# Performance work log

Measured on AMD Instinct MI355X. Metric: run time of the kernel, lower is better.

The kernel has to match this reference:

```python
import jax, jax.numpy as jnp
import numpy as np

B, C, H, W = 8, 96, 256, 256
PATCH, DIM, HEAD = 2, 384, 4
D = DIM // HEAD          # 96, minGRU feature dim
K = 2 * PATCH + 1        # 5, patch-embed kernel
GK = 3                   # positional conv kernel


def setup_inputs() -> dict:
    key = jax.random.key(0)
    ks = jax.random.split(key, 16)
    w = lambda k, shape: jax.random.normal(k, shape, jnp.float32) * 0.02
    return {
        'x': jax.random.normal(ks[0], (B, C, H, W), jnp.float32),
        'r_pw': w(ks[1], (DIM, C, K, K)),            # Conv2d weight (out,in,kh,kw)
        'r_pb': w(ks[2], (DIM,)),
        'c_pw': w(ks[3], (DIM, C, K, K)),
        'c_pb': w(ks[4], (DIM,)),
        'r_pe_w': w(ks[5], (DIM, DIM // C, GK, GK)),  # grouped conv, groups=C
        'r_pe_b': w(ks[6], (DIM,)),
        'c_pe_w': w(ks[7], (DIM, DIM // C, GK, GK)),
        'c_pe_b': w(ks[8], (DIM,)),
        'r_un_w': w(ks[9], (DIM, C, PATCH, PATCH)),   # ConvTranspose2d weight (in,out,kh,kw)
        'r_un_b': w(ks[10], (C,)),
        'c_un_w': w(ks[11], (DIM, C, PATCH, PATCH)),
        'c_un_b': w(ks[12], (C,)),
        'r_gru_w': w(ks[13], (D, 2 * D)),             # minGRU to_hidden_and_gate (no bias)
        'c_gru_w': w(ks[14], (D, 2 * D)),
    }


def _conv(x, w, b, stride, pad, groups=1):
    y = jax.lax.conv_general_dilated(
        x, w, (stride, stride), [(pad, pad), (pad, pad)],
        dimension_numbers=('NCHW', 'OIHW', 'NCHW'), feature_group_count=groups)
    return y + b[None, :, None, None]


def _min_gru(seq, w):
    # seq: (N, S, D); log-space parallel scan (heinsen scan), lucidrains minGRU
    hg = seq @ w                                  # (N, S, 2D)
    hidden, gate = jnp.split(hg, 2, axis=-1)
    log_coeffs = -jax.nn.softplus(gate)           # log(1 - z)
    log_z = -jax.nn.softplus(-gate)               # log z
    log_tilde_h = jnp.where(hidden >= 0,
                            jnp.log(jax.nn.relu(hidden) + 0.5),
                            -jax.nn.softplus(-hidden))
    a_star = jnp.cumsum(log_coeffs, axis=1)
    log_h = a_star + jax.lax.cumlogsumexp(log_z + log_tilde_h - a_star, axis=1)
    return jnp.exp(log_h)


def _unpatch(x, w, b):
    # ConvTranspose2d with kernel==stride==PATCH, pad=0: pure block expansion
    Bq, Ci, Hp, Wp = x.shape
    y = jnp.einsum('bchw,copq->bohpwq', x, w).reshape(Bq, w.shape[1], Hp * PATCH, Wp * PATCH)
    return y + b[None, :, None, None]


def reference(x, r_pw, r_pb, c_pw, c_pb, r_pe_w, r_pe_b, c_pe_w, c_pe_b,
              r_un_w, r_un_b, c_un_w, c_un_b, r_gru_w, c_gru_w):
    r = _conv(x, r_pw, r_pb, PATCH, PATCH)        # (B, DIM, Hp, Wp)
    c = _conv(x, c_pw, c_pb, PATCH, PATCH)
    r_pe = _conv(r, r_pe_w, r_pe_b, 1, 1, groups=C)
    c_pe = _conv(c, c_pe_w, c_pe_b, 1, 1, groups=C)
    Bq, _, Hp, Wp = r.shape
    # row scan: (B,head,D,Hp,Wp) -> (B,head,Wp,Hp,D) -> scan over Hp
    r = r.reshape(Bq, HEAD, D, Hp, Wp).transpose(0, 1, 4, 3, 2).reshape(-1, Hp, D)
    # col scan: (B,head,D,Hp,Wp) -> (B,head,Hp,Wp,D) -> scan over Wp
    c = c.reshape(Bq, HEAD, D, Hp, Wp).transpose(0, 1, 3, 4, 2).reshape(-1, Wp, D)
    r = _min_gru(r, r_gru_w)
    c = _min_gru(c, c_gru_w)
    r = r.reshape(Bq, HEAD, Wp, Hp, D).transpose(0, 1, 4, 3, 2).reshape(Bq, DIM, Hp, Wp)
    c = c.reshape(Bq, HEAD, Hp, Wp, D).transpose(0, 1, 4, 2, 3).reshape(Bq, DIM, Hp, Wp)
    return _unpatch(r + r_pe, r_un_w, r_un_b) + _unpatch(c + c_pe, c_un_w, c_un_b)
```

## Files before the change

kernel.cpp:

```cpp
#include <hip/hip_runtime.h>
#include <stdint.h>
#include <stdio.h>

typedef __attribute__((ext_vector_type(8))) short short8;
typedef __attribute__((ext_vector_type(4))) float f32x4;
typedef __attribute__((ext_vector_type(2))) float f32x2;
typedef __attribute__((ext_vector_type(4))) unsigned int u32x4;
typedef __attribute__((ext_vector_type(4))) unsigned short u16x4;

#define DEV static __device__ __forceinline__

DEV unsigned short f2bf(float f){
  unsigned u = __float_as_uint(f);
  u += 0x7FFFu + ((u >> 16) & 1u);
  return (unsigned short)(u >> 16);
}
DEV float bf2f(unsigned short h){ return __uint_as_float(((unsigned)h) << 16); }

__global__ __launch_bounds__(256) void k_xt(const float* __restrict__ x,
                                            unsigned short* __restrict__ xt){
  int bid = blockIdx.x;
  int wq = bid & 3, h = (bid >> 2) & 255, b = bid >> 10;
  int w0 = wq * 64;
  __shared__ unsigned short s[64 * 104];
  int t = threadIdx.x;
  int wl = t & 63, cq = t >> 6;
  const float* xp = x + ((size_t)b * 96 * 256 + h) * 256 + w0 + wl;
  #pragma unroll
  for (int i = 0; i < 24; ++i){
    int c = cq + i * 4;
    s[wl * 104 + c] = f2bf(xp[(size_t)c * 65536]);
  }
  __syncthreads();
  unsigned short* dst = xt + (((size_t)b * 260 + h + 2) * 260 + (w0 + 2)) * 128;
  #pragma unroll
  for (int p = 0; p < 3; ++p){
    int i = t + p * 256;
    int w = i / 12, ch = i % 12;
    u32x4 v = *(const u32x4*)&s[w * 104 + ch * 8];
    *(u32x4*)&dst[(size_t)w * 128 + ch * 8] = v;
  }
}

__global__ __launch_bounds__(256) void k_pack(const float* __restrict__ rpw, const float* __restrict__ cpw,
    const float* __restrict__ runw, const float* __restrict__ cunw,
    const float* __restrict__ runb, const float* __restrict__ cunb,
    const float* __restrict__ rgw,  const float* __restrict__ cgw,
    unsigned short* __restrict__ A2, unsigned short* __restrict__ Aun,
    unsigned short* __restrict__ Agr, float* __restrict__ bun){
  int tid = blockIdx.x * 256 + threadIdx.x;
  const int NA2 = 768 * 2400, NUN = 384 * 768, NGR = 2 * 192 * 96;
  if (tid < NA2){
    int oc = tid / 2400, r = tid % 2400;
    int kh = r / 480, kw = (r / 96) % 5, ic = r % 96;
    const float* W = oc < 384 ? rpw : cpw;
    int o = oc < 384 ? oc : oc - 384;
    A2[tid] = f2bf(W[(((size_t)o * 96 + ic) * 5 + kh) * 5 + kw]);
  } else if (tid < NA2 + NUN){
    int i = tid - NA2;
    int m = i / 768, ci = i % 768;
    int co = m >> 2, p = (m >> 1) & 1, q = m & 1;
    const float* W = ci < 384 ? runw : cunw;
    int c = ci < 384 ? ci : ci - 384;
    Aun[i] = f2bf(W[(((size_t)c * 96 + co) * 2 + p) * 2 + q]);
  } else if (tid < NA2 + NUN + NGR){
    int i = tid - NA2 - NUN;
    int side = i / 18432, r = i % 18432;
    int m = r / 96, k = r % 96;
    const float* W = side ? cgw : rgw;
    Agr[i] = f2bf(W[k * 192 + m]);
  } else if (tid < NA2 + NUN + NGR + 96){
    int co = tid - NA2 - NUN - NGR;
    bun[co] = runb[co] + cunb[co];
  }
}

__global__ __launch_bounds__(512) void k_conv(const unsigned short* __restrict__ xt,
    const unsigned short* __restrict__ A2,
    const float* __restrict__ rpb, const float* __restrict__ cpb,
    unsigned short* __restrict__ cl){
  __shared__ char lds[160768];
  const int BOFF = 26624;
  const int BPITCH = 33536;
  const int BITEMS = 8384;
  int t = threadIdx.x, lane = t & 63;
  int wid = t >> 6, mw = wid >> 2, nw = wid & 3;
  int wl = lane & 15, cg = lane >> 4;
  int bid = blockIdx.x;
  int xcd = bid & 7, rr = bid >> 3;
  int mt = rr % 6, pgrp = rr / 6;
  int p = pgrp * 8 + xcd;
  int wq = p & 1, hq = (p >> 1) & 31, b = p >> 6;
  int ho0 = hq * 4, wo0 = wq * 64;
  int M0 = mt * 128;

  int a_oc = t >> 2, a_q = t & 3;
  const unsigned short* Aoc = A2 + (size_t)(M0 + a_oc) * 2400 + a_q * 24;
  char* Adst = lds + a_oc * 208 + a_q * 48;

  f32x4 acc[4][4];
  #pragma unroll
  for (int i = 0; i < 4; ++i)
    #pragma unroll
    for (int j = 0; j < 4; ++j) acc[i][j] = (f32x4){0.f, 0.f, 0.f, 0.f};

  u32x4 aR[3], bR[17];
  #pragma unroll
  for (int c = 0; c < 3; ++c) aR[c] = *(const u32x4*)(Aoc + c * 8);
  #pragma unroll
  for (int it = 0; it < 17; ++it){
    int i = t + it * 512;
    if (i < BITEMS){
      int row = i / 2096, j = i % 2096, col = j >> 4, ch = j & 15;
      bR[it] = *(const u32x4*)&xt[(((size_t)b * 260 + 2 * ho0 + 2 * row) * 260 + 2 * wo0 + col) * 128 + ch * 8];
    }
  }
  #pragma unroll
  for (int c = 0; c < 3; ++c) *(u32x4*)(Adst + c * 16) = aR[c];
  #pragma unroll
  for (int it = 0; it < 17; ++it){
    int i = t + it * 512;
    if (i < BITEMS){
      int row = i / 2096, j = i % 2096, col = j >> 4, ch = j & 15;
      *(u32x4*)(lds + BOFF + row * BPITCH + col * 256 + (ch ^ ((col >> 1) & 7)) * 16) = bR[it];
    }
  }
  __syncthreads();

  for (int kh = 0; kh < 5; ++kh){
    #pragma unroll
    for (int kw = 0; kw < 5; ++kw){
      bool last = (kh == 4 && kw == 4);
      bool khb  = (kw == 4 && kh < 4);
      if (!last){
        int nkh = kh + (kw == 4 ? 1 : 0), nkw = (kw == 4 ? 0 : kw + 1);
        const unsigned short* As = Aoc + (nkh * 5 + nkw) * 96;
        #pragma unroll
        for (int c = 0; c < 3; ++c) aR[c] = *(const u32x4*)(As + c * 8);
      }
      if (khb){
        #pragma unroll
        for (int it = 0; it < 17; ++it){
          int i = t + it * 512;
          if (i < BITEMS){
            int row = i / 2096, j = i % 2096, col = j >> 4, ch = j & 15;
            bR[it] = *(const u32x4*)&xt[(((size_t)b * 260 + 2 * ho0 + 2 * row + kh + 1) * 260 + 2 * wo0 + col) * 128 + ch * 8];
          }
        }
      }
      {
        int col = 32 * nw + 2 * wl + kw;
        int sx = (col >> 1) & 7;
        #pragma unroll
        for (int ics = 0; ics < 3; ++ics){
          short8 af[4], bfr[4];
          #pragma unroll
          for (int mf = 0; mf < 4; ++mf)
            af[mf] = *(const short8*)(lds + (mw * 64 + mf * 16 + wl) * 208 + ics * 64 + cg * 16);
          int chl = (ics * 4 + cg) ^ sx;
          #pragma unroll
          for (int nf = 0; nf < 4; ++nf)
            bfr[nf] = *(const short8*)(lds + BOFF + nf * BPITCH + col * 256 + chl * 16);
          #pragma unroll
          for (int mf = 0; mf < 4; ++mf)
            #pragma unroll
            for (int nf = 0; nf < 4; ++nf)
              acc[mf][nf] = __builtin_amdgcn_mfma_f32_16x16x32_bf16(af[mf], bfr[nf], acc[mf][nf], 0, 0, 0);
        }
      }
      __syncthreads();
      if (!last){
        #pragma unroll
        for (int c = 0; c < 3; ++c) *(u32x4*)(Adst + c * 16) = aR[c];
        if (khb){
          #pragma unroll
          for (int it = 0; it < 17; ++it){
            int i = t + it * 512;
            if (i < BITEMS){
              int row = i / 2096, j = i % 2096, col = j >> 4, ch = j & 15;
              *(u32x4*)(lds + BOFF + row * BPITCH + col * 256 + (ch ^ ((col >> 1) & 7)) * 16) = bR[it];
            }
          }
        }
      }
      __syncthreads();
    }
  }
  unsigned short* S = (unsigned short*)lds;
  #pragma unroll
  for (int mf = 0; mf < 4; ++mf)
    #pragma unroll
    for (int nf = 0; nf < 4; ++nf){
      int wol = nw * 16 + wl;
      int pxl = nf * 64 + wol;
      int sw8 = (pxl & 7) << 3;
      #pragma unroll
      for (int j = 0; j < 4; ++j){
        int ocl = mw * 64 + mf * 16 + cg * 4 + j;
        int oc = M0 + ocl;
        float v = acc[mf][nf][j] + (oc < 384 ? rpb[oc] : cpb[oc - 384]);
        S[pxl * 128 + (ocl ^ sw8)] = f2bf(v);
      }
    }
  __syncthreads();
  #pragma unroll
  for (int it = 0; it < 8; ++it){
    int i = t + it * 512;
    int pxl = i >> 4, ch = i & 15;
    int chs = ch ^ (pxl & 7);
    int ho = ho0 + (pxl >> 6), wo = wo0 + (pxl & 63);
    u32x4 v = *(const u32x4*)&S[pxl * 128 + chs * 8];
    *(u32x4*)&cl[(((size_t)b * 128 + ho) * 128 + wo) * 768 + M0 + ch * 8] = v;
  }
}

__global__ __launch_bounds__(256) void k_pe(const unsigned short* __restrict__ cl,
    const float* __restrict__ rpew, const float* __restrict__ cpew,
    const float* __restrict__ rpeb, const float* __restrict__ cpeb,
    unsigned short* __restrict__ sum){
  __shared__ unsigned short si[340 * 52];
  __shared__ float sw[48 * 36];
  __shared__ float sb[48];
  int bid = blockIdx.x;
  int wq = bid & 3, hq = (bid >> 2) & 15, slab = (bid >> 6) & 15, b = bid >> 10;
  int ch0 = slab * 48, hp0 = hq * 8, wp0 = wq * 32;
  int t = threadIdx.x;
  for (int i = t; i < 48 * 36; i += 256){
    int ocl = i / 36, r = i % 36;
    int oc = ch0 + ocl;
    const float* W = oc < 384 ? rpew : cpew;
    int o = oc < 384 ? oc : oc - 384;
    sw[i] = W[(size_t)o * 36 + r];
  }
  if (t < 48){
    int oc = ch0 + t;
    sb[t] = oc < 384 ? rpeb[oc] : cpeb[oc - 384];
  }
  for (int i = t; i < 340 * 24; i += 256){
    int pix = i / 24, c2 = i % 24;
    int r2 = pix / 34, cc = pix % 34;
    int hp = hp0 - 1 + r2, wp = wp0 - 1 + cc;
    unsigned v = 0;
    if (hp >= 0 && hp < 128 && wp >= 0 && wp < 128)
      v = *(const unsigned*)&cl[((size_t)b * 16384 + hp * 128 + wp) * 768 + ch0 + c2 * 2];
    *(unsigned*)&si[pix * 52 + c2 * 2] = v;
  }
  __syncthreads();
  int hpl = t >> 5, wpl = t & 31;
  unsigned int outp[24];
  #pragma unroll
  for (int g = 0; g < 12; ++g){
    float o0 = sb[g * 4], o1 = sb[g * 4 + 1], o2 = sb[g * 4 + 2], o3 = sb[g * 4 + 3];
    #pragma unroll
    for (int dh = 0; dh < 3; ++dh)
      #pragma unroll
      for (int dw = 0; dw < 3; ++dw){
        int pix = (hpl + dh) * 34 + (wpl + dw);
        u16x4 v = *(const u16x4*)&si[pix * 52 + g * 4];
        float x0 = bf2f(v[0]), x1 = bf2f(v[1]), x2 = bf2f(v[2]), x3 = bf2f(v[3]);
        int r = dh * 3 + dw;
        o0 = fmaf(sw[(g*4+0)*36 + 0*9 + r], x0, o0); o0 = fmaf(sw[(g*4+0)*36 + 1*9 + r], x1, o0);
        o0 = fmaf(sw[(g*4+0)*36 + 2*9 + r], x2, o0); o0 = fmaf(sw[(g*4+0)*36 + 3*9 + r], x3, o0);
        o1 = fmaf(sw[(g*4+1)*36 + 0*9 + r], x0, o1); o1 = fmaf(sw[(g*4+1)*36 + 1*9 + r], x1, o1);
        o1 = fmaf(sw[(g*4+1)*36 + 2*9 + r], x2, o1); o1 = fmaf(sw[(g*4+1)*36 + 3*9 + r], x3, o1);
        o2 = fmaf(sw[(g*4+2)*36 + 0*9 + r], x0, o2); o2 = fmaf(sw[(g*4+2)*36 + 1*9 + r], x1, o2);
        o2 = fmaf(sw[(g*4+2)*36 + 2*9 + r], x2, o2); o2 = fmaf(sw[(g*4+2)*36 + 3*9 + r], x3, o2);
        o3 = fmaf(sw[(g*4+3)*36 + 0*9 + r], x0, o3); o3 = fmaf(sw[(g*4+3)*36 + 1*9 + r], x1, o3);
        o3 = fmaf(sw[(g*4+3)*36 + 2*9 + r], x2, o3); o3 = fmaf(sw[(g*4+3)*36 + 3*9 + r], x3, o3);
      }
    outp[g * 2]     = (unsigned)f2bf(o0) | ((unsigned)f2bf(o1) << 16);
    outp[g * 2 + 1] = (unsigned)f2bf(o2) | ((unsigned)f2bf(o3) << 16);
  }
  size_t obase = (((size_t)b * 128 + hp0 + hpl) * 128 + wp0 + wpl) * 768 + ch0;
  #pragma unroll
  for (int c6 = 0; c6 < 6; ++c6){
    u32x4 v = { outp[c6 * 4], outp[c6 * 4 + 1], outp[c6 * 4 + 2], outp[c6 * 4 + 3] };
    *(u32x4*)&sum[obase + c6 * 8] = v;
  }
}

__global__ __launch_bounds__(256) void k_gruf(const unsigned short* __restrict__ cl,
    const unsigned short* __restrict__ Agr, unsigned short* __restrict__ sum){
  __shared__ char lds[78848];
  const int AOFF = 0, BOFF2 = 39936, HOFF = 53248;
  int t = threadIdx.x, lane = t & 63, wid = t >> 6;
  int wl = lane & 15, cg = lane >> 4;
  int bid = blockIdx.x;
  int cb = bid & 7, head = (bid >> 3) & 3, b = (bid >> 5) & 7, side = bid >> 8;
  size_t clbase = ((size_t)b * 16384) * 768 + side * 384 + head * 96;
  for (int i = t; i < 2304; i += 256){
    int m = i / 12, c = i % 12;
    u32x4 v = *(const u32x4*)&Agr[((size_t)side * 192 + m) * 96 + c * 8];
    *(u32x4*)(lds + AOFF + m * 208 + c * 16) = v;
  }
  for (int i = t; i < 768; i += 256){
    int px = i / 12, c = i % 12;
    int s = px >> 4, xl = px & 15;
    int xg = cb * 16 + xl;
    int pxg = side ? (xg * 128 + s) : (s * 128 + xg);
    u32x4 v = *(const u32x4*)&cl[clbase + (size_t)pxg * 768 + c * 8];
    *(u32x4*)(lds + BOFF2 + px * 208 + c * 16) = v;
  }
  int s_chain = t & 15, s_dg = t >> 4;
  float h[8];
  #pragma unroll
  for (int k = 0; k < 8; ++k) h[k] = 0.f;
  __syncthreads();

  for (int ch = 0; ch < 32; ++ch){
    int s0 = ch * 4;
    f32x4 acc[12];
    #pragma unroll
    for (int i = 0; i < 12; ++i) acc[i] = (f32x4){0.f, 0.f, 0.f, 0.f};
    #pragma unroll
    for (int ks = 0; ks < 3; ++ks){
      short8 bf = *(const short8*)(lds + BOFF2 + (wid * 16 + wl) * 208 + ks * 64 + cg * 16);
      #pragma unroll
      for (int mf = 0; mf < 12; ++mf){
        short8 af = *(const short8*)(lds + AOFF + (mf * 16 + wl) * 208 + ks * 64 + cg * 16);
        acc[mf] = __builtin_amdgcn_mfma_f32_16x16x32_bf16(af, bf, acc[mf], 0, 0, 0);
      }
    }
    {
      int px = wid * 16 + wl;
      #pragma unroll
      for (int mf = 0; mf < 12; ++mf){
        unsigned p0 = (unsigned)f2bf(acc[mf][0]) | ((unsigned)f2bf(acc[mf][1]) << 16);
        unsigned p1 = (unsigned)f2bf(acc[mf][2]) | ((unsigned)f2bf(acc[mf][3]) << 16);
        unsigned long long pp = (unsigned long long)p0 | ((unsigned long long)p1 << 32);
        *(unsigned long long*)(lds + HOFF + px * 400 + (mf * 16 + cg * 4) * 2) = pp;
      }
    }
    __syncthreads();
    if (s_dg < 12){
      #pragma unroll
      for (int s = 0; s < 4; ++s){
        int px = s * 16 + s_chain;
        short8 hid8 = *(const short8*)(lds + HOFF + px * 400 + s_dg * 16);
        short8 gat8 = *(const short8*)(lds + HOFF + px * 400 + 192 + s_dg * 16);
        int xg = cb * 16 + s_chain;
        int pxg = side ? (xg * 128 + (s0 + s)) : ((s0 + s) * 128 + xg);
        unsigned short* sp = (unsigned short*)&sum[clbase + (size_t)pxg * 768 + s_dg * 8];
        u32x4 sv = *(u32x4*)sp;
        unsigned short* svp = (unsigned short*)&sv;
        #pragma unroll
        for (int k = 0; k < 8; ++k){
          float hid = bf2f((unsigned short)hid8[k]);
          float gat = bf2f((unsigned short)gat8[k]);
          float z  = 1.f / (1.f + __expf(-gat));
          float th = hid >= 0.f ? hid + 0.5f : 1.f / (1.f + __expf(-hid));
          h[k] += z * (th - h[k]);
          svp[k] = f2bf(bf2f(svp[k]) + h[k]);
        }
        *(u32x4*)sp = sv;
      }
    }
    if (ch < 31){
      int sn = (ch + 1) * 4;
      for (int i = t; i < 768; i += 256){
        int px = i / 12, c = i % 12;
        int s = px >> 4, xl = px & 15;
        int xg = cb * 16 + xl;
        int pxg = side ? (xg * 128 + (sn + s)) : ((sn + s) * 128 + xg);
        u32x4 v = *(const u32x4*)&cl[clbase + (size_t)pxg * 768 + c * 8];
        *(u32x4*)(lds + BOFF2 + px * 208 + c * 16) = v;
      }
    }
    __syncthreads();
  }
}

__global__ __launch_bounds__(256) void k_unpatch(const unsigned short* __restrict__ sum,
    const unsigned short* __restrict__ Aun, const float* __restrict__ bun,
    float* __restrict__ out){
  __shared__ char lds[53248];
  int t = threadIdx.x, lane = t & 63;
  int wid = t >> 6, mw = wid >> 1, nw = wid & 1;
  int bid = blockIdx.x;
  int xcd = bid & 7, rr = bid >> 3;
  int mt = rr % 3, pgrp = rr / 3;
  int M0 = mt * 128;
  size_t N0 = (size_t)(pgrp * 8 + xcd) * 128;
  f32x4 acc[4][4];
  #pragma unroll
  for (int i = 0; i < 4; ++i)
    #pragma unroll
    for (int j = 0; j < 4; ++j) acc[i][j] = (f32x4){0.f, 0.f, 0.f, 0.f};
  for (int kc = 0; kc < 8; ++kc){
    __syncthreads();
    for (int i = t; i < 1536; i += 256){
      int m = i / 12, c = i % 12;
      u32x4 v = *(const u32x4*)&Aun[(size_t)(M0 + m) * 768 + kc * 96 + c * 8];
      *(u32x4*)(lds + m * 208 + c * 16) = v;
    }
    for (int i = t; i < 1536; i += 256){
      int px = i / 12, c = i % 12;
      u32x4 v = *(const u32x4*)&sum[(N0 + px) * 768 + kc * 96 + c * 8];
      *(u32x4*)(lds + 26624 + px * 208 + c * 16) = v;
    }
    __syncthreads();
    #pragma unroll
    for (int ks = 0; ks < 3; ++ks){
      short8 af[4], bfr[4];
      #pragma unroll
      for (int mf = 0; mf < 4; ++mf)
        af[mf] = *(const short8*)(lds + (mw * 64 + mf * 16 + (lane & 15)) * 208 + ks * 64 + (lane >> 4) * 16);
      #pragma unroll
      for (int nf = 0; nf < 4; ++nf)
        bfr[nf] = *(const short8*)(lds + 26624 + (nw * 64 + nf * 16 + (lane & 15)) * 208 + ks * 64 + (lane >> 4) * 16);
      #pragma unroll
      for (int mf = 0; mf < 4; ++mf)
        #pragma unroll
        for (int nf = 0; nf < 4; ++nf)
          acc[mf][nf] = __builtin_amdgcn_mfma_f32_16x16x32_bf16(af[mf], bfr[nf], acc[mf][nf], 0, 0, 0);
    }
  }
  #pragma unroll
  for (int mf = 0; mf < 4; ++mf)
    #pragma unroll
    for (int nf = 0; nf < 4; ++nf){
      int m = M0 + mw * 64 + mf * 16 + (lane >> 4) * 4;
      int co = m >> 2;
      size_t px = N0 + nw * 64 + nf * 16 + (lane & 15);
      int b = (int)(px >> 14); int pxl = (int)(px & 16383);
      int hp = pxl >> 7, wp = pxl & 127;
      float bias = bun[co];
      f32x2 v01 = { acc[mf][nf][0] + bias, acc[mf][nf][1] + bias };
      f32x2 v23 = { acc[mf][nf][2] + bias, acc[mf][nf][3] + bias };
      size_t ob = (((size_t)b * 96 + co) * 256 + 2 * hp) * 256 + 2 * wp;
      *(f32x2*)&out[ob]       = v01;
      *(f32x2*)&out[ob + 256] = v23;
    }
}

extern "C" void kernel_launch(void* const* d_in, const int* in_sizes, int n_in,
                              void* d_out, int out_size, void* d_ws, size_t ws_size,
                              hipStream_t stream){
  (void)in_sizes; (void)n_in; (void)out_size;
  const float* x    = (const float*)d_in[0];
  const float* rpw  = (const float*)d_in[1];
  const float* rpb  = (const float*)d_in[2];
  const float* cpw  = (const float*)d_in[3];
  const float* cpb  = (const float*)d_in[4];
  const float* rpew = (const float*)d_in[5];
  const float* rpeb = (const float*)d_in[6];
  const float* cpew = (const float*)d_in[7];
  const float* cpeb = (const float*)d_in[8];
  const float* runw = (const float*)d_in[9];
  const float* runb = (const float*)d_in[10];
  const float* cunw = (const float*)d_in[11];
  const float* cunb = (const float*)d_in[12];
  const float* rgw  = (const float*)d_in[13];
  const float* cgw  = (const float*)d_in[14];

  char* ws = (char*)d_ws;
  const size_t SZ_XT   = (size_t)8 * 260 * 260 * 128 * 2;
  const size_t OFF_A2  = SZ_XT;
  const size_t SZ_A2   = (size_t)768 * 2400 * 2;
  const size_t OFF_AUN = OFF_A2 + SZ_A2;
  const size_t SZ_AUN  = (size_t)384 * 768 * 2;
  const size_t OFF_AGR = OFF_AUN + SZ_AUN;
  const size_t SZ_AGR  = (size_t)2 * 192 * 96 * 2;
  const size_t OFF_BUN = OFF_AGR + SZ_AGR;
  const size_t OFF_HG  = ((OFF_BUN + 384) + 255) & ~(size_t)255;
  const size_t SZ_PL   = (size_t)8 * 768 * 128 * 128 * 2;
  const size_t OFF_CL  = OFF_HG + SZ_PL;
  const size_t OFF_SUM = OFF_CL + SZ_PL;
  const size_t NEED    = OFF_SUM + SZ_PL;
  if (ws_size < NEED){
    fprintf(stderr, "kernel_launch: ws_size %zu < needed %zu\n", ws_size, NEED);
    return;
  }
  unsigned short* xt  = (unsigned short*)(ws);
  unsigned short* A2  = (unsigned short*)(ws + OFF_A2);
  unsigned short* Aun = (unsigned short*)(ws + OFF_AUN);
  unsigned short* Agr = (unsigned short*)(ws + OFF_AGR);
  float*          bun = (float*)(ws + OFF_BUN);
  unsigned short* cl  = (unsigned short*)(ws + OFF_CL);
  unsigned short* sum = (unsigned short*)(ws + OFF_SUM);
  float* out = (float*)d_out;

  hipMemsetAsync(xt, 0, SZ_XT, stream);
  k_xt  <<<dim3(8192),    dim3(256), 0, stream>>>(x, xt);
  k_pack<<<dim3(8497),    dim3(256), 0, stream>>>(rpw, cpw, runw, cunw, runb, cunb, rgw, cgw, A2, Aun, Agr, bun);
  k_conv<<<dim3(3072),    dim3(512), 0, stream>>>(xt, A2, rpb, cpb, cl);
  k_pe  <<<dim3(8192),    dim3(256), 0, stream>>>(cl, rpew, cpew, rpeb, cpeb, sum);
  k_gruf<<<dim3(512),     dim3(256), 0, stream>>>(cl, Agr, sum);
  k_unpatch<<<dim3(3072), dim3(256), 0, stream>>>(sum, Aun, bun, out);
}
```

Baseline: 1.688 ms.

## Double-buffer conv weight tile, shrink B tile to 96 channels, prefetch scan inputs

The patch-embed conv kernel now keeps two LDS copies of the weight tile and alternates between them. This cuts per-tap synchronisation from two barriers to one, and only the kernel-row boundary needs the extra barrier. The input tile now stores just the 96 real channels per column with a 208-byte pitch instead of 128 padded channels with an XOR swizzle, which reduces global loads and LDS footprint but may bring back bank conflicts. In the scan kernel, the next chunk's input loads are issued into registers before the recurrence step, so their latency overlaps the scan arithmetic.

```diff
diff --git a/kernel.cpp b/kernel.cpp
--- a/kernel.cpp
+++ b/kernel.cpp
@@ -79,10 +79,11 @@
     const unsigned short* __restrict__ A2,
     const float* __restrict__ rpb, const float* __restrict__ cpb,
     unsigned short* __restrict__ cl){
-  __shared__ char lds[160768];
-  const int BOFF = 26624;
-  const int BPITCH = 33536;
-  const int BITEMS = 8384;
+  __shared__ char lds[162240];
+  const int ASZ = 26624;
+  const int BOFF = 53248;
+  const int BPITCH = 27248;
+  const int BITEMS = 6288;
   int t = threadIdx.x, lane = t & 63;
   int wid = t >> 6, mw = wid >> 2, nw = wid & 3;
   int wl = lane & 15, cg = lane >> 4;
@@ -104,29 +105,30 @@
     #pragma unroll
     for (int j = 0; j < 4; ++j) acc[i][j] = (f32x4){0.f, 0.f, 0.f, 0.f};
 
-  u32x4 aR[3], bR[17];
+  u32x4 aR[3], bR[13];
   #pragma unroll
   for (int c = 0; c < 3; ++c) aR[c] = *(const u32x4*)(Aoc + c * 8);
   #pragma unroll
-  for (int it = 0; it < 17; ++it){
+  for (int it = 0; it < 13; ++it){
     int i = t + it * 512;
     if (i < BITEMS){
-      int row = i / 2096, j = i % 2096, col = j >> 4, ch = j & 15;
+      int row = i / 1572, j = i % 1572, col = j / 12, ch = j % 12;
       bR[it] = *(const u32x4*)&xt[(((size_t)b * 260 + 2 * ho0 + 2 * row) * 260 + 2 * wo0 + col) * 128 + ch * 8];
     }
   }
   #pragma unroll
   for (int c = 0; c < 3; ++c) *(u32x4*)(Adst + c * 16) = aR[c];
   #pragma unroll
-  for (int it = 0; it < 17; ++it){
+  for (int it = 0; it < 13; ++it){
     int i = t + it * 512;
     if (i < BITEMS){
-      int row = i / 2096, j = i % 2096, col = j >> 4, ch = j & 15;
-      *(u32x4*)(lds + BOFF + row * BPITCH + col * 256 + (ch ^ ((col >> 1) & 7)) * 16) = bR[it];
+      int row = i / 1572, j = i % 1572, col = j / 12, ch = j % 12;
+      *(u32x4*)(lds + BOFF + row * BPITCH + col * 208 + ch * 16) = bR[it];
     }
   }
   __syncthreads();
 
+  int cur = 0;
   for (int kh = 0; kh < 5; ++kh){
     #pragma unroll
     for (int kw = 0; kw < 5; ++kw){
@@ -140,27 +142,26 @@
       }
       if (khb){
         #pragma unroll
-        for (int it = 0; it < 17; ++it){
+        for (int it = 0; it < 13; ++it){
           int i = t + it * 512;
           if (i < BITEMS){
-            int row = i / 2096, j = i % 2096, col = j >> 4, ch = j & 15;
+            int row = i / 1572, j = i % 1572, col = j / 12, ch = j % 12;
             bR[it] = *(const u32x4*)&xt[(((size_t)b * 260 + 2 * ho0 + 2 * row + kh + 1) * 260 + 2 * wo0 + col) * 128 + ch * 8];
           }
         }
       }
       {
+        char* Ab = lds + cur * ASZ;
         int col = 32 * nw + 2 * wl + kw;
-        int sx = (col >> 1) & 7;
         #pragma unroll
         for (int ics = 0; ics < 3; ++ics){
           short8 af[4], bfr[4];
           #pragma unroll
           for (int mf = 0; mf < 4; ++mf)
-            af[mf] = *(const short8*)(lds + (mw * 64 + mf * 16 + wl) * 208 + ics * 64 + cg * 16);
-          int chl = (ics * 4 + cg) ^ sx;
+            af[mf] = *(const short8*)(Ab + (mw * 64 + mf * 16 + wl) * 208 + ics * 64 + cg * 16);
           #pragma unroll
           for (int nf = 0; nf < 4; ++nf)
-            bfr[nf] = *(const short8*)(lds + BOFF + nf * BPITCH + col * 256 + chl * 16);
+            bfr[nf] = *(const short8*)(lds + BOFF + nf * BPITCH + col * 208 + (ics * 4 + cg) * 16);
           #pragma unroll
           for (int mf = 0; mf < 4; ++mf)
             #pragma unroll
@@ -168,24 +169,26 @@
               acc[mf][nf] = __builtin_amdgcn_mfma_f32_16x16x32_bf16(af[mf], bfr[nf], acc[mf][nf], 0, 0, 0);
         }
       }
-      __syncthreads();
+      if (khb) __syncthreads();
       if (!last){
         #pragma unroll
-        for (int c = 0; c < 3; ++c) *(u32x4*)(Adst + c * 16) = aR[c];
+        for (int c = 0; c < 3; ++c) *(u32x4*)(Adst + (cur ^ 1) * ASZ + c * 16) = aR[c];
         if (khb){
           #pragma unroll
-          for (int it = 0; it < 17; ++it){
+          for (int it = 0; it < 13; ++it){
             int i = t + it * 512;
             if (i < BITEMS){
-              int row = i / 2096, j = i % 2096, col = j >> 4, ch = j & 15;
-              *(u32x4*)(lds + BOFF + row * BPITCH + col * 256 + (ch ^ ((col >> 1) & 7)) * 16) = bR[it];
+              int row = i / 1572, j = i % 1572, col = j / 12, ch = j % 12;
+              *(u32x4*)(lds + BOFF + row * BPITCH + col * 208 + ch * 16) = bR[it];
             }
           }
         }
-      }
-      __syncthreads();
-    }
-  }
+        __syncthreads();
+        cur ^= 1;
+      }
+    }
+  }
+  __syncthreads();
   unsigned short* S = (unsigned short*)lds;
   #pragma unroll
   for (int mf = 0; mf < 4; ++mf)
@@ -332,6 +335,19 @@
       }
     }
     __syncthreads();
+    u32x4 nb[3];
+    if (ch < 31){
+      int sn = (ch + 1) * 4;
+      #pragma unroll
+      for (int it = 0; it < 3; ++it){
+        int i = t + it * 256;
+        int px = i / 12, c = i % 12;
+        int s = px >> 4, xl = px & 15;
+        int xg = cb * 16 + xl;
+        int pxg = side ? (xg * 128 + (sn + s)) : ((sn + s) * 128 + xg);
+        nb[it] = *(const u32x4*)&cl[clbase + (size_t)pxg * 768 + c * 8];
+      }
+    }
     if (s_dg < 12){
       #pragma unroll
       for (int s = 0; s < 4; ++s){
@@ -356,14 +372,11 @@
       }
     }
     if (ch < 31){
-      int sn = (ch + 1) * 4;
-      for (int i = t; i < 768; i += 256){
+      #pragma unroll
+      for (int it = 0; it < 3; ++it){
+        int i = t + it * 256;
         int px = i / 12, c = i % 12;
-        int s = px >> 4, xl = px & 15;
-        int xg = cb * 16 + xl;
-        int pxg = side ? (xg * 128 + (sn + s)) : ((sn + s) * 128 + xg);
-        u32x4 v = *(const u32x4*)&cl[clbase + (size_t)pxg * 768 + c * 8];
-        *(u32x4*)(lds + BOFF2 + px * 208 + c * 16) = v;
+        *(u32x4*)(lds + BOFF2 + px * 208 + c * 16) = nb[it];
       }
     }
     __syncthreads();
```

After: 1.486 ms. -12.0%, faster.
